# Kernel optimization log

Measured on AMD Instinct MI355X. Metric: run time of the kernel, lower is better.

Reference implementation:

```python
import jax, jax.numpy as jnp
import numpy as np

TOKENS, IN_DIM, HID, OUT_DIM = 32768, 256, 1024, 256
N_EXP, TOP_K = 8, 2


def setup_inputs() -> dict:
    key = jax.random.key(0)
    ks = jax.random.split(key, 6)
    s_in = 1.0 / np.sqrt(IN_DIM)
    s_hid = 1.0 / np.sqrt(HID)
    return {
        "x": jax.random.normal(ks[0], (TOKENS, IN_DIM), dtype=jnp.float32),
        "Wg": jax.random.uniform(ks[1], (IN_DIM, N_EXP), jnp.float32, -s_in, s_in),
        "W1": jax.random.uniform(ks[2], (N_EXP, IN_DIM, HID), jnp.float32, -s_in, s_in),
        "b1": jax.random.uniform(ks[3], (N_EXP, HID), jnp.float32, -s_in, s_in),
        "W2": jax.random.uniform(ks[4], (N_EXP, HID, OUT_DIM), jnp.float32, -s_hid, s_hid),
        "b2": jax.random.uniform(ks[5], (N_EXP, OUT_DIM), jnp.float32, -s_hid, s_hid),
    }


def reference(x, Wg, W1, b1, W2, b2):
    # Router: softmax over expert logits, pick top-k, renormalize weights
    logits = x @ Wg                                  # [B, E]
    router_probs = jax.nn.softmax(logits, axis=-1)   # [B, E]
    top_w, top_idx = jax.lax.top_k(router_probs, TOP_K)  # [B, K]
    top_w = top_w / jnp.sum(top_w, axis=-1, keepdims=True)
    # Dense all-expert compute (faithful to the torch.stack over experts)
    h = jax.nn.relu(jnp.einsum("bi,eih->beh", x, W1) + b1[None])   # [B, E, H]
    expert_out = jnp.einsum("beh,eho->beo", h, W2) + b2[None]       # [B, E, O]
    # Gather top-k experts per token and combine
    selected = jnp.take_along_axis(expert_out, top_idx[:, :, None], axis=1)  # [B, K, O]
    output = jnp.sum(selected * top_w[:, :, None], axis=1)                   # [B, O]
    return output, router_probs
```

## Files before the change

### kernel.cpp

```cpp
#include <hip/hip_runtime.h>
#include <hip/hip_bf16.h>
#include <stdint.h>

#define T_TOK 32768
#define IN_D  256
#define HID_D 1024
#define OUT_D 256
#define NE    8
#define BM    64
#define HC    32
#define NCH   (HID_D / HC)

typedef unsigned short u16;
typedef __attribute__((ext_vector_type(8))) __bf16 bf16x8;
typedef __attribute__((ext_vector_type(4))) float f32x4;
typedef __attribute__((ext_vector_type(4))) unsigned int u32x4;
typedef __attribute__((ext_vector_type(2))) unsigned int u32x2;

__device__ __forceinline__ u16 f2bf(float f) {
  unsigned int u = __builtin_bit_cast(unsigned int, f);
  u = (u + 0x7FFFu + ((u >> 16) & 1u)) >> 16;
  return (u16)u;
}

__device__ __forceinline__ void gload_lds16(const u16* g, u16* l) {
  __builtin_amdgcn_global_load_lds(
      (const __attribute__((address_space(1))) unsigned int*)g,
      (__attribute__((address_space(3))) unsigned int*)l, 16, 0, 0);
}

__global__ __launch_bounds__(64) void pack_w1_kernel(const float* __restrict__ W1,
                                                     u16* __restrict__ w1p) {
  int b = blockIdx.x;
  int f = b & 15, c = (b >> 4) & 31, e = b >> 9;
  int l = threadIdx.x, l15 = l & 15, l4 = l >> 4;
  int h = c * 32 + (f >> 3) * 16 + l15;
  int k0 = (f & 7) * 32 + l4 * 8;
  unsigned int w[4];
#pragma unroll
  for (int p = 0; p < 4; ++p) {
    u16 a = f2bf(W1[((size_t)e * IN_D + k0 + 2 * p) * HID_D + h]);
    u16 bq = f2bf(W1[((size_t)e * IN_D + k0 + 2 * p + 1) * HID_D + h]);
    w[p] = (unsigned int)a | ((unsigned int)bq << 16);
  }
  *reinterpret_cast<u32x4*>(w1p + (size_t)b * 512 + l * 8) = u32x4{w[0], w[1], w[2], w[3]};
}

__global__ __launch_bounds__(64) void pack_w2_kernel(const float* __restrict__ W2,
                                                     u16* __restrict__ w2p) {
  int b = blockIdx.x;
  int f = b & 15, c = (b >> 4) & 31, e = b >> 9;
  int l = threadIdx.x, l15 = l & 15, l4 = l >> 4;
  int o = f * 16 + l15;
  int k0 = c * 32 + l4 * 8;
  unsigned int w[4];
#pragma unroll
  for (int p = 0; p < 4; ++p) {
    u16 a = f2bf(W2[((size_t)e * HID_D + k0 + 2 * p) * OUT_D + o]);
    u16 bq = f2bf(W2[((size_t)e * HID_D + k0 + 2 * p + 1) * OUT_D + o]);
    w[p] = (unsigned int)a | ((unsigned int)bq << 16);
  }
  *reinterpret_cast<u32x4*>(w2p + (size_t)b * 512 + l * 8) = u32x4{w[0], w[1], w[2], w[3]};
}

__global__ __launch_bounds__(256) void router_kernel(
    const float* __restrict__ x, const float* __restrict__ Wg,
    u16* __restrict__ xbf, float* __restrict__ probs, int* __restrict__ counts,
    int* __restrict__ list_tok, float* __restrict__ list_w) {
  __shared__ float wg_s[IN_D * NE];
  __shared__ int lcnt[NE];
  __shared__ int gbase[NE];
  int tid = threadIdx.x;
  for (int i = tid; i < IN_D * NE; i += 256) wg_s[i] = Wg[i];
  if (tid < NE) lcnt[tid] = 0;
  __syncthreads();

  int lane = tid & 63;
  int wave = tid >> 6;
  int q = lane & 3;
  int tk = blockIdx.x * 64 + wave * 16 + (lane >> 2);

  float acc[NE];
#pragma unroll
  for (int e = 0; e < NE; ++e) acc[e] = 0.f;
  const float* xrow = x + (size_t)tk * IN_D;
  u16* xbrow = xbf + (size_t)tk * IN_D;
#pragma unroll
  for (int i = 0; i < 16; ++i) {
    int c = i * 4 + q;
    f32x4 v = *reinterpret_cast<const f32x4*>(xrow + c * 4);
    unsigned int lo = (unsigned int)f2bf(v[0]) | ((unsigned int)f2bf(v[1]) << 16);
    unsigned int hi = (unsigned int)f2bf(v[2]) | ((unsigned int)f2bf(v[3]) << 16);
    *reinterpret_cast<u32x2*>(xbrow + c * 4) = u32x2{lo, hi};
#pragma unroll
    for (int j = 0; j < 4; ++j) {
      const float* wr = &wg_s[(c * 4 + j) * NE];
#pragma unroll
      for (int e = 0; e < NE; ++e) acc[e] = fmaf(v[j], wr[e], acc[e]);
    }
  }
#pragma unroll
  for (int e = 0; e < NE; ++e) {
    acc[e] += __shfl_xor(acc[e], 1);
    acc[e] += __shfl_xor(acc[e], 2);
  }
  float m = acc[0];
#pragma unroll
  for (int e = 1; e < NE; ++e) m = fmaxf(m, acc[e]);
  float p[NE], s = 0.f;
#pragma unroll
  for (int e = 0; e < NE; ++e) { p[e] = expf(acc[e] - m); s += p[e]; }
  float inv = 1.f / s;
#pragma unroll
  for (int e = 0; e < NE; ++e) p[e] *= inv;
  int i0 = 0; float p0 = p[0];
#pragma unroll
  for (int e = 1; e < NE; ++e) if (p[e] > p0) { p0 = p[e]; i0 = e; }
  int i1 = -1; float p1 = -1.f;
#pragma unroll
  for (int e = 0; e < NE; ++e) if (e != i0 && p[e] > p1) { p1 = p[e]; i1 = e; }
  float wsum = p0 + p1;

  int lp0 = 0, lp1 = 0;
  if (q == 0) {
    *reinterpret_cast<f32x4*>(probs + (size_t)tk * NE)     = f32x4{p[0], p[1], p[2], p[3]};
    *reinterpret_cast<f32x4*>(probs + (size_t)tk * NE + 4) = f32x4{p[4], p[5], p[6], p[7]};
    lp0 = atomicAdd(&lcnt[i0], 1);
    lp1 = atomicAdd(&lcnt[i1], 1);
  }
  __syncthreads();
  if (tid < NE) gbase[tid] = atomicAdd(&counts[tid], lcnt[tid]);
  __syncthreads();
  if (q == 0) {
    int e0 = gbase[i0] + lp0;
    list_tok[(size_t)i0 * T_TOK + e0] = tk;
    list_w[(size_t)i0 * T_TOK + e0] = p0 / wsum;
    int e1 = gbase[i1] + lp1;
    list_tok[(size_t)i1 * T_TOK + e1] = tk | (1 << 16);
    list_w[(size_t)i1 * T_TOK + e1] = p1 / wsum;
  }
}

__global__ __launch_bounds__(512, 4) void moe_main_kernel(
    const u16* __restrict__ xbf, const u16* __restrict__ w1p,
    const u16* __restrict__ w2p, const float* __restrict__ b1,
    const float* __restrict__ b2, const int* __restrict__ counts,
    const int* __restrict__ list_tok, const float* __restrict__ list_w,
    float* __restrict__ part) {
  int e = blockIdx.x & 7;
  int tile = blockIdx.x >> 3;
  int cnt = counts[e];
  int base = tile * BM;
  if (base >= cnt) return;

  __shared__ __align__(16) u16 W1s[2][16 * 512];
  __shared__ __align__(16) u16 Hs[2][4 * 512];
  __shared__ float Bs[HID_D];
  __shared__ int toks[BM];
  __shared__ float gw[BM];

  int tid = threadIdx.x;
  int wave = tid >> 6;
  int lane = tid & 63;
  const int l15 = lane & 15;
  const int l4 = lane >> 4;
  const int hh = wave & 1;
  const int tt = wave >> 1;

  if (tid < BM) {
    int idx = base + tid;
    int tv = 0; float w = 0.f;
    if (idx < cnt) { tv = list_tok[(size_t)e * T_TOK + idx]; w = list_w[(size_t)e * T_TOK + idx]; }
    toks[tid] = tv;
    gw[tid] = w;
  }
#pragma unroll
  for (int j = 0; j < 2; ++j) Bs[tid + j * 512] = b1[(size_t)e * HID_D + tid + j * 512];

  const u16* w1base = w1p + (size_t)e * NCH * 16 * 512;
  const u16* w2base = w2p + (size_t)e * NCH * 16 * 512;

  auto stage = [&](int c, int buf) {
#pragma unroll
    for (int j2 = 0; j2 < 2; ++j2) {
      int f = wave * 2 + j2;
      gload_lds16(w1base + ((size_t)c * 16 + f) * 512 + lane * 8, &W1s[buf][f * 512]);
    }
  };
  auto loadW2 = [&](int c, u32x4* w2r) {
#pragma unroll
    for (int of = 0; of < 2; ++of)
      w2r[of] = *reinterpret_cast<const u32x4*>(
          w2base + ((size_t)c * 16 + wave * 2 + of) * 512 + lane * 8);
  };

  stage(0, 0);
  __syncthreads();

  u32x4 bx[8];
  {
    const u16* xr = xbf + (size_t)(toks[tt * 16 + l15] & 0xFFFF) * IN_D + l4 * 8;
#pragma unroll
    for (int kk = 0; kk < 8; ++kk)
      bx[kk] = __builtin_nontemporal_load(reinterpret_cast<const u32x4*>(xr + kk * 32));
  }

  u32x4 w2A[2], w2B[2];
  f32x4 acc[2][4];
#pragma unroll
  for (int a = 0; a < 2; ++a)
#pragma unroll
    for (int b = 0; b < 4; ++b) acc[a][b] = f32x4{0.f, 0.f, 0.f, 0.f};

  auto p1 = [&](int c, int wb, int hb) {
    f32x4 accH = f32x4{0.f, 0.f, 0.f, 0.f};
#pragma unroll
    for (int kk = 0; kk < 8; ++kk) {
      const char* pa = reinterpret_cast<const char*>(&W1s[wb][0]) +
                       (hh * 8 + kk) * 1024 + lane * 16;
      bf16x8 a = __builtin_bit_cast(bf16x8, *reinterpret_cast<const u32x4*>(pa));
      accH = __builtin_amdgcn_mfma_f32_16x16x32_bf16(a, __builtin_bit_cast(bf16x8, bx[kk]), accH, 0, 0, 0);
    }
    f32x4 bias = *reinterpret_cast<const f32x4*>(&Bs[c * HC + hh * 16 + l4 * 4]);
    u16 q0 = f2bf(fmaxf(accH[0] + bias[0], 0.f));
    u16 q1 = f2bf(fmaxf(accH[1] + bias[1], 0.f));
    u16 q2 = f2bf(fmaxf(accH[2] + bias[2], 0.f));
    u16 q3 = f2bf(fmaxf(accH[3] + bias[3], 0.f));
    unsigned int lo = (unsigned int)q0 | ((unsigned int)q1 << 16);
    unsigned int hi = (unsigned int)q2 | ((unsigned int)q3 << 16);
    char* p = reinterpret_cast<char*>(&Hs[hb][0]) + tt * 1024 +
              ((hh * 2 + (l4 >> 1)) * 16 + l15) * 16 + (l4 & 1) * 8;
    *reinterpret_cast<u32x2*>(p) = u32x2{lo, hi};
  };

  auto p2 = [&](int hb, const u32x4* w2r) {
    bf16x8 bh[4];
#pragma unroll
    for (int tf = 0; tf < 4; ++tf)
      bh[tf] = __builtin_bit_cast(bf16x8, *reinterpret_cast<const u32x4*>(
          reinterpret_cast<const char*>(&Hs[hb][0]) + tf * 1024 + lane * 16));
#pragma unroll
    for (int of = 0; of < 2; ++of) {
      bf16x8 a = __builtin_bit_cast(bf16x8, w2r[of]);
#pragma unroll
      for (int tf = 0; tf < 4; ++tf)
        acc[of][tf] = __builtin_amdgcn_mfma_f32_16x16x32_bf16(a, bh[tf], acc[of][tf], 0, 0, 0);
    }
  };

  loadW2(0, w2A);
  p1(0, 0, 0);
  stage(1, 1);
  loadW2(1, w2B);
  asm volatile("s_waitcnt vmcnt(0) lgkmcnt(0)" ::: "memory");
  __builtin_amdgcn_s_barrier();

#pragma unroll 1
  for (int c = 1; c < NCH; c += 2) {
    if (c + 1 < NCH) stage(c + 1, 0);
    p2(0, w2A);
    if (c + 1 < NCH) loadW2(c + 1, w2A);
    p1(c, 1, 1);
    asm volatile("s_waitcnt vmcnt(0) lgkmcnt(0)" ::: "memory");
    __builtin_amdgcn_s_barrier();
    if (c + 1 < NCH) {
      if (c + 2 < NCH) stage(c + 2, 1);
      p2(1, w2B);
      if (c + 2 < NCH) loadW2(c + 2, w2B);
      p1(c + 1, 0, 0);
      asm volatile("s_waitcnt vmcnt(0) lgkmcnt(0)" ::: "memory");
      __builtin_amdgcn_s_barrier();
    }
  }
  p2(1, w2B);

#pragma unroll
  for (int of = 0; of < 2; ++of) {
    int ob = (wave * 2 + of) * 16 + l4 * 4;
    f32x4 bv = *reinterpret_cast<const f32x4*>(b2 + (size_t)e * OUT_D + ob);
#pragma unroll
    for (int tf = 0; tf < 4; ++tf) {
      int trow = tf * 16 + l15;
      if (base + trow < cnt) {
        int tv = toks[trow];
        int tok = tv & 0xFFFF;
        int slot = tv >> 16;
        float w = gw[trow];
        f32x4 o;
#pragma unroll
        for (int r = 0; r < 4; ++r) o[r] = w * (acc[of][tf][r] + bv[r]);
        __builtin_nontemporal_store(
            o, reinterpret_cast<f32x4*>(part + ((size_t)slot * T_TOK + tok) * OUT_D + ob));
      }
    }
  }
}

__global__ __launch_bounds__(256) void combine_kernel(const float* __restrict__ part,
                                                      float* __restrict__ out) {
  size_t i = (size_t)blockIdx.x * 256 + threadIdx.x;
  f32x4 a = __builtin_nontemporal_load(reinterpret_cast<const f32x4*>(part) + i);
  f32x4 b = __builtin_nontemporal_load(
      reinterpret_cast<const f32x4*>(part + (size_t)T_TOK * OUT_D) + i);
  f32x4 o = a + b;
  __builtin_nontemporal_store(o, reinterpret_cast<f32x4*>(out) + i);
}

extern "C" void kernel_launch(void* const* d_in, const int* in_sizes, int n_in,
                              void* d_out, int out_size, void* d_ws, size_t ws_size,
                              hipStream_t stream) {
  const float* x  = (const float*)d_in[0];
  const float* Wg = (const float*)d_in[1];
  const float* W1 = (const float*)d_in[2];
  const float* b1 = (const float*)d_in[3];
  const float* W2 = (const float*)d_in[4];
  const float* b2 = (const float*)d_in[5];
  float* out = (float*)d_out;

  char* ws = (char*)d_ws;
  constexpr size_t OFF_XBF  = 0;
  constexpr size_t OFF_W1P  = (size_t)T_TOK * IN_D * 2;
  constexpr size_t OFF_W2P  = OFF_W1P + (size_t)NE * HID_D * IN_D * 2;
  constexpr size_t OFF_CNT  = OFF_W2P + (size_t)NE * OUT_D * HID_D * 2;
  constexpr size_t OFF_LTOK = OFF_CNT + 128;
  constexpr size_t OFF_LW   = OFF_LTOK + (size_t)NE * T_TOK * 4;
  constexpr size_t OFF_PART = OFF_LW + (size_t)NE * T_TOK * 4;

  u16*   xbf      = (u16*)(ws + OFF_XBF);
  u16*   w1p      = (u16*)(ws + OFF_W1P);
  u16*   w2p      = (u16*)(ws + OFF_W2P);
  int*   counts   = (int*)(ws + OFF_CNT);
  int*   list_tok = (int*)(ws + OFF_LTOK);
  float* list_w   = (float*)(ws + OFF_LW);
  float* part     = (float*)(ws + OFF_PART);
  float* probs    = out + (size_t)T_TOK * OUT_D;

  hipMemsetAsync(counts, 0, NE * sizeof(int), stream);

  pack_w1_kernel<<<NE * NCH * 16, 64, 0, stream>>>(W1, w1p);
  pack_w2_kernel<<<NE * NCH * 16, 64, 0, stream>>>(W2, w2p);
  router_kernel<<<T_TOK / 64, 256, 0, stream>>>(x, Wg, xbf, probs, counts,
                                                list_tok, list_w);

  moe_main_kernel<<<(T_TOK / BM) * NE, 512, 0, stream>>>(
      xbf, w1p, w2p, b1, b2, counts, list_tok, list_w, part);

  combine_kernel<<<(T_TOK * OUT_D / 4) / 256, 256, 0, stream>>>(part, out);
}
```

Baseline: 161.3 us.

## Store expert partials in bf16, reshape W2 wave tiling, add setprio, batch pack blocks

The per-slot expert partial outputs are now stored as bf16 instead of fp32, which halves the scatter writes and the combine reads. The combine kernel widens each bf16 pair to float before summing. The second-GEMM wave mapping changes from 2 output fragments × 4 token fragments to 4 × 2, and a single W2 register set is reloaded each chunk instead of double-buffering two sets. s_setprio is placed around the MFMA loops, and the pack kernels now run 4 waves per block. Rounding partials to bf16 adds precision loss, and loading W2 just before use may expose global-load latency.

```diff
diff --git a/kernel.cpp b/kernel.cpp
--- a/kernel.cpp
+++ b/kernel.cpp
@@ -29,11 +29,11 @@
       (__attribute__((address_space(3))) unsigned int*)l, 16, 0, 0);
 }
 
-__global__ __launch_bounds__(64) void pack_w1_kernel(const float* __restrict__ W1,
-                                                     u16* __restrict__ w1p) {
-  int b = blockIdx.x;
+__global__ __launch_bounds__(256) void pack_w1_kernel(const float* __restrict__ W1,
+                                                      u16* __restrict__ w1p) {
+  int b = blockIdx.x * 4 + (threadIdx.x >> 6);
   int f = b & 15, c = (b >> 4) & 31, e = b >> 9;
-  int l = threadIdx.x, l15 = l & 15, l4 = l >> 4;
+  int l = threadIdx.x & 63, l15 = l & 15, l4 = l >> 4;
   int h = c * 32 + (f >> 3) * 16 + l15;
   int k0 = (f & 7) * 32 + l4 * 8;
   unsigned int w[4];
@@ -46,11 +46,11 @@
   *reinterpret_cast<u32x4*>(w1p + (size_t)b * 512 + l * 8) = u32x4{w[0], w[1], w[2], w[3]};
 }
 
-__global__ __launch_bounds__(64) void pack_w2_kernel(const float* __restrict__ W2,
-                                                     u16* __restrict__ w2p) {
-  int b = blockIdx.x;
+__global__ __launch_bounds__(256) void pack_w2_kernel(const float* __restrict__ W2,
+                                                      u16* __restrict__ w2p) {
+  int b = blockIdx.x * 4 + (threadIdx.x >> 6);
   int f = b & 15, c = (b >> 4) & 31, e = b >> 9;
-  int l = threadIdx.x, l15 = l & 15, l4 = l >> 4;
+  int l = threadIdx.x & 63, l15 = l & 15, l4 = l >> 4;
   int o = f * 16 + l15;
   int k0 = c * 32 + l4 * 8;
   unsigned int w[4];
@@ -146,7 +146,7 @@
     const u16* __restrict__ w2p, const float* __restrict__ b1,
     const float* __restrict__ b2, const int* __restrict__ counts,
     const int* __restrict__ list_tok, const float* __restrict__ list_w,
-    float* __restrict__ part) {
+    u16* __restrict__ part) {
   int e = blockIdx.x & 7;
   int tile = blockIdx.x >> 3;
   int cnt = counts[e];
@@ -166,6 +166,8 @@
   const int l4 = lane >> 4;
   const int hh = wave & 1;
   const int tt = wave >> 1;
+  const int wo = wave & 3;
+  const int wt = wave >> 2;
 
   if (tid < BM) {
     int idx = base + tid;
@@ -189,9 +191,9 @@
   };
   auto loadW2 = [&](int c, u32x4* w2r) {
 #pragma unroll
-    for (int of = 0; of < 2; ++of)
+    for (int of = 0; of < 4; ++of)
       w2r[of] = *reinterpret_cast<const u32x4*>(
-          w2base + ((size_t)c * 16 + wave * 2 + of) * 512 + lane * 8);
+          w2base + ((size_t)c * 16 + wo * 4 + of) * 512 + lane * 8);
   };
 
   stage(0, 0);
@@ -205,15 +207,16 @@
       bx[kk] = __builtin_nontemporal_load(reinterpret_cast<const u32x4*>(xr + kk * 32));
   }
 
-  u32x4 w2A[2], w2B[2];
-  f32x4 acc[2][4];
-#pragma unroll
-  for (int a = 0; a < 2; ++a)
-#pragma unroll
-    for (int b = 0; b < 4; ++b) acc[a][b] = f32x4{0.f, 0.f, 0.f, 0.f};
+  u32x4 w2r[4];
+  f32x4 acc[4][2];
+#pragma unroll
+  for (int a = 0; a < 4; ++a)
+#pragma unroll
+    for (int b = 0; b < 2; ++b) acc[a][b] = f32x4{0.f, 0.f, 0.f, 0.f};
 
   auto p1 = [&](int c, int wb, int hb) {
     f32x4 accH = f32x4{0.f, 0.f, 0.f, 0.f};
+    __builtin_amdgcn_s_setprio(1);
 #pragma unroll
     for (int kk = 0; kk < 8; ++kk) {
       const char* pa = reinterpret_cast<const char*>(&W1s[wb][0]) +
@@ -221,6 +224,7 @@
       bf16x8 a = __builtin_bit_cast(bf16x8, *reinterpret_cast<const u32x4*>(pa));
       accH = __builtin_amdgcn_mfma_f32_16x16x32_bf16(a, __builtin_bit_cast(bf16x8, bx[kk]), accH, 0, 0, 0);
     }
+    __builtin_amdgcn_s_setprio(0);
     f32x4 bias = *reinterpret_cast<const f32x4*>(&Bs[c * HC + hh * 16 + l4 * 4]);
     u16 q0 = f2bf(fmaxf(accH[0] + bias[0], 0.f));
     u16 q1 = f2bf(fmaxf(accH[1] + bias[1], 0.f));
@@ -233,77 +237,94 @@
     *reinterpret_cast<u32x2*>(p) = u32x2{lo, hi};
   };
 
-  auto p2 = [&](int hb, const u32x4* w2r) {
-    bf16x8 bh[4];
-#pragma unroll
-    for (int tf = 0; tf < 4; ++tf)
+  auto p2 = [&](int hb) {
+    bf16x8 bh[2];
+#pragma unroll
+    for (int tf = 0; tf < 2; ++tf)
       bh[tf] = __builtin_bit_cast(bf16x8, *reinterpret_cast<const u32x4*>(
-          reinterpret_cast<const char*>(&Hs[hb][0]) + tf * 1024 + lane * 16));
-#pragma unroll
-    for (int of = 0; of < 2; ++of) {
+          reinterpret_cast<const char*>(&Hs[hb][0]) + (wt * 2 + tf) * 1024 + lane * 16));
+    __builtin_amdgcn_s_setprio(1);
+#pragma unroll
+    for (int of = 0; of < 4; ++of) {
       bf16x8 a = __builtin_bit_cast(bf16x8, w2r[of]);
 #pragma unroll
-      for (int tf = 0; tf < 4; ++tf)
+      for (int tf = 0; tf < 2; ++tf)
         acc[of][tf] = __builtin_amdgcn_mfma_f32_16x16x32_bf16(a, bh[tf], acc[of][tf], 0, 0, 0);
     }
+    __builtin_amdgcn_s_setprio(0);
   };
 
-  loadW2(0, w2A);
+  loadW2(0, w2r);
   p1(0, 0, 0);
   stage(1, 1);
-  loadW2(1, w2B);
   asm volatile("s_waitcnt vmcnt(0) lgkmcnt(0)" ::: "memory");
   __builtin_amdgcn_s_barrier();
 
 #pragma unroll 1
   for (int c = 1; c < NCH; c += 2) {
     if (c + 1 < NCH) stage(c + 1, 0);
-    p2(0, w2A);
-    if (c + 1 < NCH) loadW2(c + 1, w2A);
+    p2(0);
+    loadW2(c, w2r);
     p1(c, 1, 1);
     asm volatile("s_waitcnt vmcnt(0) lgkmcnt(0)" ::: "memory");
     __builtin_amdgcn_s_barrier();
     if (c + 1 < NCH) {
       if (c + 2 < NCH) stage(c + 2, 1);
-      p2(1, w2B);
-      if (c + 2 < NCH) loadW2(c + 2, w2B);
+      p2(1);
+      loadW2(c + 1, w2r);
       p1(c + 1, 0, 0);
       asm volatile("s_waitcnt vmcnt(0) lgkmcnt(0)" ::: "memory");
       __builtin_amdgcn_s_barrier();
     }
   }
-  p2(1, w2B);
-
-#pragma unroll
-  for (int of = 0; of < 2; ++of) {
-    int ob = (wave * 2 + of) * 16 + l4 * 4;
+  p2(1);
+
+#pragma unroll
+  for (int of = 0; of < 4; ++of) {
+    int ob = (wo * 4 + of) * 16 + l4 * 4;
     f32x4 bv = *reinterpret_cast<const f32x4*>(b2 + (size_t)e * OUT_D + ob);
 #pragma unroll
-    for (int tf = 0; tf < 4; ++tf) {
-      int trow = tf * 16 + l15;
+    for (int tf = 0; tf < 2; ++tf) {
+      int trow = (wt * 2 + tf) * 16 + l15;
       if (base + trow < cnt) {
         int tv = toks[trow];
         int tok = tv & 0xFFFF;
         int slot = tv >> 16;
         float w = gw[trow];
-        f32x4 o;
-#pragma unroll
-        for (int r = 0; r < 4; ++r) o[r] = w * (acc[of][tf][r] + bv[r]);
+        u16 q0 = f2bf(w * (acc[of][tf][0] + bv[0]));
+        u16 q1 = f2bf(w * (acc[of][tf][1] + bv[1]));
+        u16 q2 = f2bf(w * (acc[of][tf][2] + bv[2]));
+        u16 q3 = f2bf(w * (acc[of][tf][3] + bv[3]));
+        unsigned int lo = (unsigned int)q0 | ((unsigned int)q1 << 16);
+        unsigned int hi = (unsigned int)q2 | ((unsigned int)q3 << 16);
+        u32x2 o2{lo, hi};
         __builtin_nontemporal_store(
-            o, reinterpret_cast<f32x4*>(part + ((size_t)slot * T_TOK + tok) * OUT_D + ob));
+            o2, reinterpret_cast<u32x2*>(part + ((size_t)slot * T_TOK + tok) * OUT_D + ob));
       }
     }
   }
 }
 
-__global__ __launch_bounds__(256) void combine_kernel(const float* __restrict__ part,
+__global__ __launch_bounds__(256) void combine_kernel(const u16* __restrict__ part,
                                                       float* __restrict__ out) {
   size_t i = (size_t)blockIdx.x * 256 + threadIdx.x;
-  f32x4 a = __builtin_nontemporal_load(reinterpret_cast<const f32x4*>(part) + i);
-  f32x4 b = __builtin_nontemporal_load(
-      reinterpret_cast<const f32x4*>(part + (size_t)T_TOK * OUT_D) + i);
-  f32x4 o = a + b;
-  __builtin_nontemporal_store(o, reinterpret_cast<f32x4*>(out) + i);
+  u32x4 a = __builtin_nontemporal_load(reinterpret_cast<const u32x4*>(part) + i);
+  u32x4 b = __builtin_nontemporal_load(
+      reinterpret_cast<const u32x4*>(part + (size_t)T_TOK * OUT_D) + i);
+  f32x4 o0, o1;
+#pragma unroll
+  for (int j = 0; j < 4; ++j) {
+    unsigned int ua = a[j], ub = b[j];
+    float a0 = __builtin_bit_cast(float, (ua & 0xFFFFu) << 16);
+    float a1 = __builtin_bit_cast(float, ua & 0xFFFF0000u);
+    float b0 = __builtin_bit_cast(float, (ub & 0xFFFFu) << 16);
+    float b1 = __builtin_bit_cast(float, ub & 0xFFFF0000u);
+    if (j < 2) { o0[j * 2] = a0 + b0; o0[j * 2 + 1] = a1 + b1; }
+    else       { o1[(j - 2) * 2] = a0 + b0; o1[(j - 2) * 2 + 1] = a1 + b1; }
+  }
+  f32x4* dst = reinterpret_cast<f32x4*>(out) + i * 2;
+  __builtin_nontemporal_store(o0, dst);
+  __builtin_nontemporal_store(o1, dst + 1);
 }
 
 extern "C" void kernel_launch(void* const* d_in, const int* in_sizes, int n_in,
@@ -332,18 +353,18 @@
   int*   counts   = (int*)(ws + OFF_CNT);
   int*   list_tok = (int*)(ws + OFF_LTOK);
   float* list_w   = (float*)(ws + OFF_LW);
-  float* part     = (float*)(ws + OFF_PART);
+  u16*   part     = (u16*)(ws + OFF_PART);
   float* probs    = out + (size_t)T_TOK * OUT_D;
 
   hipMemsetAsync(counts, 0, NE * sizeof(int), stream);
 
-  pack_w1_kernel<<<NE * NCH * 16, 64, 0, stream>>>(W1, w1p);
-  pack_w2_kernel<<<NE * NCH * 16, 64, 0, stream>>>(W2, w2p);
+  pack_w1_kernel<<<NE * NCH * 16 / 4, 256, 0, stream>>>(W1, w1p);
+  pack_w2_kernel<<<NE * NCH * 16 / 4, 256, 0, stream>>>(W2, w2p);
   router_kernel<<<T_TOK / 64, 256, 0, stream>>>(x, Wg, xbf, probs, counts,
                                                 list_tok, list_w);
 
   moe_main_kernel<<<(T_TOK / BM) * NE, 512, 0, stream>>>(
       xbf, w1p, w2p, b1, b2, counts, list_tok, list_w, part);
 
-  combine_kernel<<<(T_TOK * OUT_D / 4) / 256, 256, 0, stream>>>(part, out);
-}
+  combine_kernel<<<(T_TOK * OUT_D / 8) / 256, 256, 0, stream>>>(part, out);
+}
```

Result: slower. 171.1 us (+6.1%).
